# Performance work log

Hardware: AMD Instinct MI355X
Metric: run time of the kernel (lower is better)

Reference implementation:

```python
import jax, jax.numpy as jnp
import numpy as np

N, IN_DIM, LAT, K = 32768, 128, 64, 8192
BETA = 1.25


def _linear_params(key, d_in, d_out):
    kw, kb = jax.random.split(key)
    lim = 1.0 / np.sqrt(d_in)
    W = jax.random.uniform(kw, (d_out, d_in), minval=-lim, maxval=lim, dtype=jnp.float32)
    b = jax.random.uniform(kb, (d_out,), minval=-lim, maxval=lim, dtype=jnp.float32)
    return W, b


def setup_inputs() -> dict:
    key = jax.random.key(0)
    ks = jax.random.split(key, 9)
    x = jax.random.normal(ks[0], (N, IN_DIM), dtype=jnp.float32)
    # encoder: 128 -> 256 -> 128 -> 64
    enc_W1, enc_b1 = _linear_params(ks[1], IN_DIM, 256)
    enc_W2, enc_b2 = _linear_params(ks[2], 256, 128)
    enc_W3, enc_b3 = _linear_params(ks[3], 128, LAT)
    # codebook: uniform(-1/K, 1/K)
    emb = jax.random.uniform(ks[4], (K, LAT), minval=-1.0 / K, maxval=1.0 / K, dtype=jnp.float32)
    # decoder: 64 -> 128 -> 256 -> (mu: 128, log_var: 128)
    dec_W1, dec_b1 = _linear_params(ks[5], LAT, 128)
    dec_W2, dec_b2 = _linear_params(ks[6], 128, 256)
    dec_Wmu, dec_bmu = _linear_params(ks[7], 256, IN_DIM)
    dec_Wlv, dec_blv = _linear_params(ks[8], 256, IN_DIM)
    return {
        'x': x,
        'enc_W1': enc_W1, 'enc_b1': enc_b1,
        'enc_W2': enc_W2, 'enc_b2': enc_b2,
        'enc_W3': enc_W3, 'enc_b3': enc_b3,
        'emb': emb,
        'dec_W1': dec_W1, 'dec_b1': dec_b1,
        'dec_W2': dec_W2, 'dec_b2': dec_b2,
        'dec_Wmu': dec_Wmu, 'dec_bmu': dec_bmu,
        'dec_Wlv': dec_Wlv, 'dec_blv': dec_blv,
    }


def reference(x, enc_W1, enc_b1, enc_W2, enc_b2, enc_W3, enc_b3, emb,
              dec_W1, dec_b1, dec_W2, dec_b2, dec_Wmu, dec_bmu, dec_Wlv, dec_blv):
    sg = jax.lax.stop_gradient
    # encoder MLP
    h = jax.nn.relu(x @ enc_W1.T + enc_b1)
    h = jax.nn.relu(h @ enc_W2.T + enc_b2)
    lat = h @ enc_W3.T + enc_b3                      # [N, D]
    # vector quantizer: [N, K] pairwise squared distances
    d = (jnp.sum(lat * lat, axis=1, keepdims=True)
         + jnp.sum(emb * emb, axis=1)
         - 2.0 * lat @ emb.T)
    inds = jnp.argmin(d, axis=1)                     # [N]
    one_hot = jax.nn.one_hot(inds, K, dtype=jnp.float32)   # [N, K]
    q = emb[inds]                                    # gather == one_hot @ emb
    commitment = jnp.mean((sg(q) - lat) ** 2)
    embedding_loss = jnp.mean((q - sg(lat)) ** 2)
    vq_loss = BETA * commitment + embedding_loss
    z = lat + sg(q - lat)                            # straight-through
    # decoder MLP
    h = jax.nn.relu(z @ dec_W1.T + dec_b1)
    h = jax.nn.relu(h @ dec_W2.T + dec_b2)
    x_hat = h @ dec_Wmu.T + dec_bmu
    x_hat_var = h @ dec_Wlv.T + dec_blv
    return x_hat, x_hat_var, one_hot, vq_loss
```

## Files before the change

kernel.cpp:

```cpp
#include <hip/hip_runtime.h>
#include <cfloat>
#include <climits>

#define TPB 256


typedef float f32x4 __attribute__((ext_vector_type(4)));

__device__ __forceinline__ void nt_store4(float* p, float4 v) {
  f32x4 nv;
  nv.x = v.x; nv.y = v.y; nv.z = v.z; nv.w = v.w;
  __builtin_nontemporal_store(nv, reinterpret_cast<f32x4*>(p));
}

__global__ __launch_bounds__(TPB) void wt_kernel(
    const float* __restrict__ W1, const float* __restrict__ W2,
    const float* __restrict__ W3, const float* __restrict__ U1,
    const float* __restrict__ U2, const float* __restrict__ Umu,
    const float* __restrict__ Ulv, float* __restrict__ wt) {
  __shared__ float sB[64 * 68];
  const int b = blockIdx.x;
  const float* src; int R, C, lt; float* dst;
  if (b < 8)       { src = W1;  R = 256; C = 128; dst = wt;          lt = b; }
  else if (b < 16) { src = W2;  R = 128; C = 256; dst = wt + 32768;  lt = b - 8; }
  else if (b < 18) { src = W3;  R = 64;  C = 128; dst = wt + 65536;  lt = b - 16; }
  else if (b < 20) { src = U1;  R = 128; C = 64;  dst = wt + 73728;  lt = b - 18; }
  else if (b < 28) { src = U2;  R = 256; C = 128; dst = wt + 81920;  lt = b - 20; }
  else if (b < 36) { src = Umu; R = 128; C = 256; dst = wt + 114688; lt = b - 28; }
  else             { src = Ulv; R = 128; C = 256; dst = wt + 147456; lt = b - 36; }
  const int tiles_r = R >> 6;
  const int r0 = (lt % tiles_r) << 6, c0 = (lt / tiles_r) << 6;
  const int t = threadIdx.x;
  for (int v = t; v < 1024; v += TPB) {
    const int c4 = v & 15, r = v >> 4;
    const float4 w =
        *reinterpret_cast<const float4*>(src + (size_t)(r0 + r) * C + c0 + 4 * c4);
    *reinterpret_cast<float4*>(&sB[r * 68 + 4 * c4]) = w;
  }
  __syncthreads();
  for (int v = t; v < 1024; v += TPB) {
    const int r4 = v & 15, c = v >> 4;
    float4 o;
    o.x = sB[(4 * r4 + 0) * 68 + c];
    o.y = sB[(4 * r4 + 1) * 68 + c];
    o.z = sB[(4 * r4 + 2) * 68 + c];
    o.w = sB[(4 * r4 + 3) * 68 + c];
    *reinterpret_cast<float4*>(dst + (size_t)(c0 + c) * R + r0 + 4 * r4) = o;
  }
}

__global__ __launch_bounds__(TPB) void embt_kernel(const float* __restrict__ emb,
                                                   float* __restrict__ embT,
                                                   float* __restrict__ En) {
  __shared__ float sB[64 * 68];
  const int c0 = blockIdx.x * 64;
  const int t = threadIdx.x;
  for (int v = t; v < 1024; v += TPB) {
    const int d4 = v & 15, r = v >> 4;
    const float4 e =
        *reinterpret_cast<const float4*>(emb + (size_t)(c0 + r) * 64 + 4 * d4);
    *reinterpret_cast<float4*>(&sB[r * 68 + 4 * d4]) = e;
  }
  __syncthreads();
  if (t < 64) {
    const float* row = &sB[t * 68];
    float q[8];
#pragma unroll
    for (int j = 0; j < 8; ++j) q[j] = __fmul_rn(row[j], row[j]);
#pragma unroll
    for (int m = 1; m < 8; ++m)
#pragma unroll
      for (int j = 0; j < 8; ++j) {
        const float v = row[m * 8 + j];
        q[j] = __fadd_rn(q[j], __fmul_rn(v, v));
      }
    En[c0 + t] = __fadd_rn(
        __fadd_rn(__fadd_rn(q[0], q[1]), __fadd_rn(q[2], q[3])),
        __fadd_rn(__fadd_rn(q[4], q[5]), __fadd_rn(q[6], q[7])));
  }
  for (int v = t; v < 1024; v += TPB) {
    const int r4 = v & 15, d = v >> 4;
    float4 o;
    o.x = sB[(4 * r4 + 0) * 68 + d];
    o.y = sB[(4 * r4 + 1) * 68 + d];
    o.z = sB[(4 * r4 + 2) * 68 + d];
    o.w = sB[(4 * r4 + 3) * 68 + d];
    *reinterpret_cast<float4*>(embT + (size_t)d * 8192 + c0 + 4 * r4) = o;
  }
}

__global__ __launch_bounds__(512) void enc_fused(
    const float* __restrict__ x, const float* __restrict__ WT1,
    const float* __restrict__ WT2, const float* __restrict__ WT3,
    const float* __restrict__ b1, const float* __restrict__ b2,
    const float* __restrict__ b3, float* __restrict__ lat) {
  __shared__ float sX[128 * 68];
  __shared__ float sH1[256 * 68];
  __shared__ float sH2[128 * 68];
  const int t = threadIdx.x;
  const int m0 = blockIdx.x * 64;

  for (int v = t; v < 2048; v += 512) {
    const int k4 = v & 31, r = v >> 5;
    const float4 xv =
        *reinterpret_cast<const float4*>(x + (size_t)(m0 + r) * 128 + 4 * k4);
    float* dst = &sX[(4 * k4) * 68 + r];
    dst[0] = xv.x; dst[68] = xv.y; dst[136] = xv.z; dst[204] = xv.w;
  }
  __syncthreads();

  {
    const int cg8 = (t & 31) * 8, rg4 = (t >> 5) * 4;
    float acc[4][8] = {};
#pragma unroll 8
    for (int k = 0; k < 128; ++k) {
      const float4 a = *reinterpret_cast<const float4*>(&sX[k * 68 + rg4]);
      const float* wr = WT1 + (size_t)k * 256 + cg8;
      const float4 b0 = *reinterpret_cast<const float4*>(wr);
      const float4 b1v = *reinterpret_cast<const float4*>(wr + 4);
      const float av[4] = {a.x, a.y, a.z, a.w};
      const float bv[8] = {b0.x, b0.y, b0.z, b0.w, b1v.x, b1v.y, b1v.z, b1v.w};
#pragma unroll
      for (int i = 0; i < 4; ++i)
#pragma unroll
        for (int j = 0; j < 8; ++j) acc[i][j] = fmaf(av[i], bv[j], acc[i][j]);
    }
#pragma unroll
    for (int j = 0; j < 8; ++j) {
      const int col = cg8 + j;
      const float bj = b1[col];
#pragma unroll
      for (int i = 0; i < 4; ++i) {
        const float h = __fadd_rn(acc[i][j], bj);
        sH1[col * 68 + rg4 + i] = h > 0.f ? h : 0.f;
      }
    }
  }
  __syncthreads();

  {
    const int cg4 = (t & 31) * 4, rg4 = (t >> 5) * 4;
    float acc[4][4] = {};
#pragma unroll 8
    for (int k = 0; k < 256; ++k) {
      const float4 a = *reinterpret_cast<const float4*>(&sH1[k * 68 + rg4]);
      const float4 bb =
          *reinterpret_cast<const float4*>(WT2 + (size_t)k * 128 + cg4);
      const float av[4] = {a.x, a.y, a.z, a.w};
      const float bv[4] = {bb.x, bb.y, bb.z, bb.w};
#pragma unroll
      for (int i = 0; i < 4; ++i)
#pragma unroll
        for (int j = 0; j < 4; ++j) acc[i][j] = fmaf(av[i], bv[j], acc[i][j]);
    }
#pragma unroll
    for (int j = 0; j < 4; ++j) {
      const int col = cg4 + j;
      const float bj = b2[col];
#pragma unroll
      for (int i = 0; i < 4; ++i) {
        const float h = __fadd_rn(acc[i][j], bj);
        sH2[col * 68 + rg4 + i] = h > 0.f ? h : 0.f;
      }
    }
  }
  __syncthreads();

  {
    const int cg4 = (t & 15) * 4, rg2 = (t >> 4) * 2;
    float acc[2][4] = {};
#pragma unroll 8
    for (int k = 0; k < 128; ++k) {
      const float2 a = *reinterpret_cast<const float2*>(&sH2[k * 68 + rg2]);
      const float4 bb =
          *reinterpret_cast<const float4*>(WT3 + (size_t)k * 64 + cg4);
      const float av[2] = {a.x, a.y};
      const float bv[4] = {bb.x, bb.y, bb.z, bb.w};
#pragma unroll
      for (int i = 0; i < 2; ++i)
#pragma unroll
        for (int j = 0; j < 4; ++j) acc[i][j] = fmaf(av[i], bv[j], acc[i][j]);
    }
#pragma unroll
    for (int i = 0; i < 2; ++i) {
      float4 o;
      o.x = __fadd_rn(acc[i][0], b3[cg4 + 0]);
      o.y = __fadd_rn(acc[i][1], b3[cg4 + 1]);
      o.z = __fadd_rn(acc[i][2], b3[cg4 + 2]);
      o.w = __fadd_rn(acc[i][3], b3[cg4 + 3]);
      *reinterpret_cast<float4*>(lat + (size_t)(m0 + rg2 + i) * 64 + cg4) = o;
    }
  }
}

__global__ __launch_bounds__(512, 4) void vqdec_kernel(
    const float* __restrict__ lat, const float* __restrict__ embT,
    const float* __restrict__ En, const float* __restrict__ emb,
    const float* __restrict__ UT1, const float* __restrict__ ub1,
    const float* __restrict__ UT2, const float* __restrict__ ub2,
    const float* __restrict__ UTmu, const float* __restrict__ ubmu,
    const float* __restrict__ UTlv, const float* __restrict__ ublv,
    float* __restrict__ oh, float* __restrict__ xh, float* __restrict__ xv,
    float* __restrict__ lossp) {
  __shared__ float smem[13056];
  __shared__ float snl[64];
  __shared__ int ridx[64];
  __shared__ float lacc;
  const int t = threadIdx.x;
  const int m0 = blockIdx.x * 64;

  {
    float* const sL = smem;
    float* const sE = smem + 4352;
    const int cg = t & 31, rg = t >> 5;
    const int cg4 = cg * 4, rg4 = rg * 4;

    for (int v = t; v < 1024; v += 512) {
      const int r = v >> 4, d4 = v & 15;
      const float4 lv =
          *reinterpret_cast<const float4*>(lat + (size_t)(m0 + r) * 64 + 4 * d4);
      float* dst = &sL[(4 * d4) * 68 + r];
      dst[0] = lv.x; dst[68] = lv.y; dst[136] = lv.z; dst[204] = lv.w;
    }
    if (t == 0) lacc = 0.f;
    float4 st[4];
#pragma unroll
    for (int k = 0; k < 4; ++k) {
      const int v = t + (k << 9);
      const int d = v >> 5, c4 = v & 31;
      st[k] = *reinterpret_cast<const float4*>(embT + (size_t)d * 8192 + 4 * c4);
    }
    __syncthreads();
    if (t < 64) {
      float q[8];
#pragma unroll
      for (int j = 0; j < 8; ++j) {
        const float v = sL[j * 68 + t];
        q[j] = __fmul_rn(v, v);
      }
#pragma unroll
      for (int m = 1; m < 8; ++m)
#pragma unroll
        for (int j = 0; j < 8; ++j) {
          const float v = sL[(m * 8 + j) * 68 + t];
          q[j] = __fadd_rn(q[j], __fmul_rn(v, v));
        }
      snl[t] = __fadd_rn(
          __fadd_rn(__fadd_rn(q[0], q[1]), __fadd_rn(q[2], q[3])),
          __fadd_rn(__fadd_rn(q[4], q[5]), __fadd_rn(q[6], q[7])));
    }
    __syncthreads();
    float nl[4];
#pragma unroll
    for (int i = 0; i < 4; ++i) nl[i] = snl[rg4 + i];

    float v1[4];
    int i1[4];
#pragma unroll
    for (int i = 0; i < 4; ++i) { v1[i] = FLT_MAX; i1[i] = INT_MAX; }

    const float4 z = make_float4(0.f, 0.f, 0.f, 0.f);

    for (int ch = 0; ch < 64; ++ch) {
      const int c0 = ch << 7;
#pragma unroll
      for (int k = 0; k < 4; ++k) {
        const int v = t + (k << 9);
        const int d = v >> 5, c4 = v & 31;
        *reinterpret_cast<float4*>(&sE[d * 132 + 4 * c4]) = st[k];
      }
      __syncthreads();
#pragma unroll
      for (int k = 0; k < 4; ++k) {
        const int v = t + (k << 9);
        const int r = v >> 5, c4 = v & 31;
        nt_store4(oh + (size_t)(m0 + r) * 8192 + c0 + 4 * c4, z);
      }
      if (ch < 63) {
        const int cn = c0 + 128;
#pragma unroll
        for (int k = 0; k < 4; ++k) {
          const int v = t + (k << 9);
          const int d = v >> 5, c4 = v & 31;
          st[k] = *reinterpret_cast<const float4*>(embT + (size_t)d * 8192 +
                                                   cn + 4 * c4);
        }
      }
      const float4 EA = *reinterpret_cast<const float4*>(En + c0 + cg4);

      float acc[4][4] = {};
#pragma unroll 4
      for (int d = 0; d < 64; ++d) {
        const float4 a = *reinterpret_cast<const float4*>(&sL[d * 68 + rg4]);
        const float4 bb = *reinterpret_cast<const float4*>(&sE[d * 132 + cg4]);
        const float av[4] = {a.x, a.y, a.z, a.w};
        const float bv[4] = {bb.x, bb.y, bb.z, bb.w};
#pragma unroll
        for (int i = 0; i < 4; ++i)
#pragma unroll
          for (int j = 0; j < 4; ++j) acc[i][j] = fmaf(av[i], bv[j], acc[i][j]);
      }
      const float Ev[4] = {EA.x, EA.y, EA.z, EA.w};
#pragma unroll
      for (int j = 0; j < 4; ++j) {
        const int c = c0 + cg4 + j;
        const float Ec = Ev[j];
#pragma unroll
        for (int i = 0; i < 4; ++i) {
          const float t1 = __fadd_rn(nl[i], Ec);
          const float s = __fsub_rn(t1, __fmul_rn(2.0f, acc[i][j]));
          if (s < v1[i]) { v1[i] = s; i1[i] = c; }
        }
      }
      __syncthreads();
    }

#pragma unroll
    for (int m = 16; m >= 1; m >>= 1) {
#pragma unroll
      for (int i = 0; i < 4; ++i) {
        const float ov = __shfl_xor(v1[i], m);
        const int oi = __shfl_xor(i1[i], m);
        if (ov < v1[i] || (ov == v1[i] && oi < i1[i])) {
          v1[i] = ov; i1[i] = oi;
        }
      }
    }
    if (cg == 0) {
      float ls = 0.f;
#pragma unroll
      for (int i = 0; i < 4; ++i) {
        ridx[rg4 + i] = i1[i];
        ls += v1[i];
      }
      atomicAdd(&lacc, ls);
    }
    __syncthreads();
    if (t == 0) lossp[blockIdx.x] = lacc;

#pragma unroll
    for (int k = 0; k < 4; ++k) {
      const int v = t + (k << 9);
      const int r = v >> 5, c4 = v & 31;
      const int ind = ridx[r];
      const int g4 = ind >> 2;
      if ((g4 & 31) == c4) {
        float4 o = make_float4(0.f, 0.f, 0.f, 0.f);
        reinterpret_cast<float*>(&o)[ind & 3] = 1.f;
        nt_store4(oh + (size_t)(m0 + r) * 8192 + 4 * g4, o);
      }
    }
  }

  {
    float* const sQ = smem;
    float* const sG1 = smem + 4352;
    float* const sG2 = smem;

    for (int v = t; v < 1024; v += 512) {
      const int k4 = v & 15, r = v >> 4;
      const int id = ridx[r];
      const float4 e =
          *reinterpret_cast<const float4*>(emb + (size_t)id * 64 + 4 * k4);
      float* dst = &sQ[(4 * k4) * 68 + r];
      dst[0] = e.x; dst[68] = e.y; dst[136] = e.z; dst[204] = e.w;
    }
    __syncthreads();

    const int cg4 = (t & 31) * 4, rg4 = (t >> 5) * 4;

    {
      float acc[4][4] = {};
#pragma unroll 8
      for (int k = 0; k < 64; ++k) {
        const float4 a = *reinterpret_cast<const float4*>(&sQ[k * 68 + rg4]);
        const float4 bb =
            *reinterpret_cast<const float4*>(UT1 + (size_t)k * 128 + cg4);
        const float av[4] = {a.x, a.y, a.z, a.w};
        const float bv[4] = {bb.x, bb.y, bb.z, bb.w};
#pragma unroll
        for (int i = 0; i < 4; ++i)
#pragma unroll
          for (int j = 0; j < 4; ++j) acc[i][j] = fmaf(av[i], bv[j], acc[i][j]);
      }
#pragma unroll
      for (int j = 0; j < 4; ++j) {
        const int col = cg4 + j;
        const float bj = ub1[col];
#pragma unroll
        for (int i = 0; i < 4; ++i) {
          const float h = acc[i][j] + bj;
          sG1[col * 68 + rg4 + i] = h > 0.f ? h : 0.f;
        }
      }
    }
    __syncthreads();

    float accA[4][4] = {}, accB[4][4] = {};
#pragma unroll 8
    for (int k = 0; k < 128; ++k) {
      const float4 a = *reinterpret_cast<const float4*>(&sG1[k * 68 + rg4]);
      const float4 bA =
          *reinterpret_cast<const float4*>(UT2 + (size_t)k * 256 + cg4);
      const float4 bB =
          *reinterpret_cast<const float4*>(UT2 + (size_t)k * 256 + 128 + cg4);
      const float av[4] = {a.x, a.y, a.z, a.w};
      const float bAv[4] = {bA.x, bA.y, bA.z, bA.w};
      const float bBv[4] = {bB.x, bB.y, bB.z, bB.w};
#pragma unroll
      for (int i = 0; i < 4; ++i)
#pragma unroll
        for (int j = 0; j < 4; ++j) {
          accA[i][j] = fmaf(av[i], bAv[j], accA[i][j]);
          accB[i][j] = fmaf(av[i], bBv[j], accB[i][j]);
        }
    }
    __syncthreads();

#pragma unroll
    for (int j = 0; j < 4; ++j) {
      const int col = cg4 + j;
      const float bj = ub2[col];
#pragma unroll
      for (int i = 0; i < 4; ++i) {
        const float h = accA[i][j] + bj;
        sG2[col * 68 + rg4 + i] = h > 0.f ? h : 0.f;
      }
    }
    __syncthreads();

    float accH[2][4][4] = {};
#pragma unroll 8
    for (int c = 0; c < 128; ++c) {
      const float4 a = *reinterpret_cast<const float4*>(&sG2[c * 68 + rg4]);
      const float4 bm =
          *reinterpret_cast<const float4*>(UTmu + (size_t)c * 128 + cg4);
      const float4 bl =
          *reinterpret_cast<const float4*>(UTlv + (size_t)c * 128 + cg4);
      const float av[4] = {a.x, a.y, a.z, a.w};
      const float bmv[4] = {bm.x, bm.y, bm.z, bm.w};
      const float blv_[4] = {bl.x, bl.y, bl.z, bl.w};
#pragma unroll
      for (int i = 0; i < 4; ++i)
#pragma unroll
        for (int j = 0; j < 4; ++j) {
          accH[0][i][j] = fmaf(av[i], bmv[j], accH[0][i][j]);
          accH[1][i][j] = fmaf(av[i], blv_[j], accH[1][i][j]);
        }
    }
    __syncthreads();

#pragma unroll
    for (int j = 0; j < 4; ++j) {
      const int col = 128 + cg4 + j;
      const float bj = ub2[col];
#pragma unroll
      for (int i = 0; i < 4; ++i) {
        const float h = accB[i][j] + bj;
        sG2[(cg4 + j) * 68 + rg4 + i] = h > 0.f ? h : 0.f;
      }
    }
    __syncthreads();

#pragma unroll 8
    for (int c = 0; c < 128; ++c) {
      const float4 a = *reinterpret_cast<const float4*>(&sG2[c * 68 + rg4]);
      const float4 bm = *reinterpret_cast<const float4*>(
          UTmu + (size_t)(128 + c) * 128 + cg4);
      const float4 bl = *reinterpret_cast<const float4*>(
          UTlv + (size_t)(128 + c) * 128 + cg4);
      const float av[4] = {a.x, a.y, a.z, a.w};
      const float bmv[4] = {bm.x, bm.y, bm.z, bm.w};
      const float blv_[4] = {bl.x, bl.y, bl.z, bl.w};
#pragma unroll
      for (int i = 0; i < 4; ++i)
#pragma unroll
        for (int j = 0; j < 4; ++j) {
          accH[0][i][j] = fmaf(av[i], bmv[j], accH[0][i][j]);
          accH[1][i][j] = fmaf(av[i], blv_[j], accH[1][i][j]);
        }
    }

#pragma unroll
    for (int i = 0; i < 4; ++i) {
      float4 ov;
      ov.x = accH[0][i][0] + ubmu[cg4 + 0];
      ov.y = accH[0][i][1] + ubmu[cg4 + 1];
      ov.z = accH[0][i][2] + ubmu[cg4 + 2];
      ov.w = accH[0][i][3] + ubmu[cg4 + 3];
      nt_store4(xh + (size_t)(m0 + rg4 + i) * 128 + cg4, ov);
      float4 ov2;
      ov2.x = accH[1][i][0] + ublv[cg4 + 0];
      ov2.y = accH[1][i][1] + ublv[cg4 + 1];
      ov2.z = accH[1][i][2] + ublv[cg4 + 2];
      ov2.w = accH[1][i][3] + ublv[cg4 + 3];
      nt_store4(xv + (size_t)(m0 + rg4 + i) * 128 + cg4, ov2);
    }
  }
}

__global__ void fin_kernel(const float* __restrict__ lossp,
                           float* __restrict__ outp) {
  const int t = threadIdx.x;
  double s = 0.0;
  for (int i = t; i < 512; i += 64) s += (double)lossp[i];
#pragma unroll
  for (int m = 32; m >= 1; m >>= 1) s += __shfl_xor(s, m);
  if (t == 0) *outp = (float)(2.25 * s / (32768.0 * 64.0));
}

extern "C" void kernel_launch(void* const* d_in, const int* in_sizes, int n_in,
                              void* d_out, int out_size, void* d_ws,
                              size_t ws_size, hipStream_t stream) {
  const float* x = (const float*)d_in[0];
  const float* eW1 = (const float*)d_in[1];
  const float* eb1 = (const float*)d_in[2];
  const float* eW2 = (const float*)d_in[3];
  const float* eb2 = (const float*)d_in[4];
  const float* eW3 = (const float*)d_in[5];
  const float* eb3 = (const float*)d_in[6];
  const float* emb = (const float*)d_in[7];
  const float* dW1 = (const float*)d_in[8];
  const float* db1 = (const float*)d_in[9];
  const float* dW2 = (const float*)d_in[10];
  const float* db2 = (const float*)d_in[11];
  const float* dWmu = (const float*)d_in[12];
  const float* dbmu = (const float*)d_in[13];
  const float* dWlv = (const float*)d_in[14];
  const float* dblv = (const float*)d_in[15];

  float* out = (float*)d_out;
  float* xhat = out;
  float* xvar = out + 4194304;
  float* oh = out + 8388608;
  float* lossout = out + 276824064;

  float* lat = (float*)d_ws;
  float* En = lat + 2097152;
  float* lossp = En + 8192;
  int* inds = (int*)(lossp + 512);
  float* embT = (float*)(inds + 32768);
  float* wt = embT + 524288;
  float* wt1 = wt;
  float* wt2 = wt + 32768;
  float* wt3 = wt + 65536;
  float* uwt1 = wt + 73728;
  float* uwt2 = wt + 81920;
  float* uwtmu = wt + 114688;
  float* uwtlv = wt + 147456;

  wt_kernel<<<44, TPB, 0, stream>>>(eW1, eW2, eW3, dW1, dW2, dWmu, dWlv, wt);
  embt_kernel<<<128, TPB, 0, stream>>>(emb, embT, En);
  enc_fused<<<512, 512, 0, stream>>>(x, wt1, wt2, wt3, eb1, eb2, eb3, lat);
  vqdec_kernel<<<512, 512, 0, stream>>>(lat, embT, En, emb, uwt1, db1, uwt2,
                                        db2, uwtmu, dbmu, uwtlv, dblv, oh,
                                        xhat, xvar, lossp);
  fin_kernel<<<1, 64, 0, stream>>>(lossp, lossout);
}
```

Measured before the change: 833.0 us.

## Stream codebook tiles from global into registers instead of shared memory

The VQ distance loop no longer stages the codebook chunk in shared memory with per-chunk barriers. Each wavefront now covers its own 16-column slice and loads codebook values straight from global memory into a 4-deep register prefetch ring. The argmin reduction is reworked to shuffle within a wave, then combine across the 8 waves in shared memory, with a shuffle-based loss sum replacing the atomic. This removes two block barriers per chunk and the LDS store traffic. In exchange every wave issues its own global loads of the codebook, relying on cache hits, and more registers are live at once.

```diff
diff --git a/kernel.cpp b/kernel.cpp
--- a/kernel.cpp
+++ b/kernel.cpp
@@ -205,15 +205,19 @@
   __shared__ float smem[13056];
   __shared__ float snl[64];
   __shared__ int ridx[64];
-  __shared__ float lacc;
   const int t = threadIdx.x;
   const int m0 = blockIdx.x * 64;
 
   {
     float* const sL = smem;
-    float* const sE = smem + 4352;
-    const int cg = t & 31, rg = t >> 5;
-    const int cg4 = cg * 4, rg4 = rg * 4;
+    float* const sredv = smem + 4352;
+    int* const sredi = (int*)(smem + 4864);
+    const int w = t >> 6;
+    const int lane = t & 63;
+    const int rgw = lane & 15;
+    const int cgw = lane >> 4;
+    const int rg4 = rgw * 4;
+    const int cb = (w << 4) + (cgw << 2);
 
     for (int v = t; v < 1024; v += 512) {
       const int r = v >> 4, d4 = v & 15;
@@ -222,14 +226,6 @@
       float* dst = &sL[(4 * d4) * 68 + r];
       dst[0] = lv.x; dst[68] = lv.y; dst[136] = lv.z; dst[204] = lv.w;
     }
-    if (t == 0) lacc = 0.f;
-    float4 st[4];
-#pragma unroll
-    for (int k = 0; k < 4; ++k) {
-      const int v = t + (k << 9);
-      const int d = v >> 5, c4 = v & 31;
-      st[k] = *reinterpret_cast<const float4*>(embT + (size_t)d * 8192 + 4 * c4);
-    }
     __syncthreads();
     if (t < 64) {
       float q[8];
@@ -263,36 +259,28 @@
 
     for (int ch = 0; ch < 64; ++ch) {
       const int c0 = ch << 7;
-#pragma unroll
-      for (int k = 0; k < 4; ++k) {
-        const int v = t + (k << 9);
-        const int d = v >> 5, c4 = v & 31;
-        *reinterpret_cast<float4*>(&sE[d * 132 + 4 * c4]) = st[k];
-      }
-      __syncthreads();
 #pragma unroll
       for (int k = 0; k < 4; ++k) {
         const int v = t + (k << 9);
         const int r = v >> 5, c4 = v & 31;
         nt_store4(oh + (size_t)(m0 + r) * 8192 + c0 + 4 * c4, z);
       }
-      if (ch < 63) {
-        const int cn = c0 + 128;
-#pragma unroll
-        for (int k = 0; k < 4; ++k) {
-          const int v = t + (k << 9);
-          const int d = v >> 5, c4 = v & 31;
-          st[k] = *reinterpret_cast<const float4*>(embT + (size_t)d * 8192 +
-                                                   cn + 4 * c4);
-        }
-      }
-      const float4 EA = *reinterpret_cast<const float4*>(En + c0 + cg4);
+      const float4 EA = *reinterpret_cast<const float4*>(En + c0 + cb);
+
+      const float* bp = embT + c0 + cb;
+      float4 br[4];
+#pragma unroll
+      for (int p = 0; p < 4; ++p)
+        br[p] = *reinterpret_cast<const float4*>(bp + (size_t)p * 8192);
 
       float acc[4][4] = {};
 #pragma unroll 4
       for (int d = 0; d < 64; ++d) {
         const float4 a = *reinterpret_cast<const float4*>(&sL[d * 68 + rg4]);
-        const float4 bb = *reinterpret_cast<const float4*>(&sE[d * 132 + cg4]);
+        const float4 bb = br[d & 3];
+        if (d < 60)
+          br[d & 3] =
+              *reinterpret_cast<const float4*>(bp + (size_t)(d + 4) * 8192);
         const float av[4] = {a.x, a.y, a.z, a.w};
         const float bv[4] = {bb.x, bb.y, bb.z, bb.w};
 #pragma unroll
@@ -303,7 +291,7 @@
       const float Ev[4] = {EA.x, EA.y, EA.z, EA.w};
 #pragma unroll
       for (int j = 0; j < 4; ++j) {
-        const int c = c0 + cg4 + j;
+        const int c = c0 + cb + j;
         const float Ec = Ev[j];
 #pragma unroll
         for (int i = 0; i < 4; ++i) {
@@ -312,11 +300,10 @@
           if (s < v1[i]) { v1[i] = s; i1[i] = c; }
         }
       }
-      __syncthreads();
-    }
-
-#pragma unroll
-    for (int m = 16; m >= 1; m >>= 1) {
+    }
+
+#pragma unroll
+    for (int m = 16; m <= 32; m <<= 1) {
 #pragma unroll
       for (int i = 0; i < 4; ++i) {
         const float ov = __shfl_xor(v1[i], m);
@@ -326,17 +313,31 @@
         }
       }
     }
-    if (cg == 0) {
-      float ls = 0.f;
+    if (cgw == 0) {
 #pragma unroll
       for (int i = 0; i < 4; ++i) {
-        ridx[rg4 + i] = i1[i];
-        ls += v1[i];
-      }
-      atomicAdd(&lacc, ls);
-    }
-    __syncthreads();
-    if (t == 0) lossp[blockIdx.x] = lacc;
+        sredv[w * 64 + rg4 + i] = v1[i];
+        sredi[w * 64 + rg4 + i] = i1[i];
+      }
+    }
+    __syncthreads();
+
+    if (t < 64) {
+      float bv = FLT_MAX;
+      int bi = INT_MAX;
+#pragma unroll
+      for (int ww = 0; ww < 8; ++ww) {
+        const float v = sredv[ww * 64 + t];
+        const int idx = sredi[ww * 64 + t];
+        if (v < bv || (v == bv && idx < bi)) { bv = v; bi = idx; }
+      }
+      ridx[t] = bi;
+      float s = bv;
+#pragma unroll
+      for (int m = 32; m >= 1; m >>= 1) s += __shfl_xor(s, m);
+      if (t == 0) lossp[blockIdx.x] = s;
+    }
+    __syncthreads();
 
 #pragma unroll
     for (int k = 0; k < 4; ++k) {
```

New measurement: 915.7 us (median of 2 runs). 9.9% more time.
